# Kernel tuning notes

Measured on AMD Instinct MI355X. Metric: run time of the kernel, lower is better.

## Reference

```python
import jax, jax.numpy as jnp
import numpy as np

GRID_SIZE = 5
SPLINE_ORDER = 3
GRID_RANGE = (-1.0, 1.0)


def _make_grid():
    # knots: arange(-k, grid_size + k + 1) * h + lo -> 12 points for k=3, g=5
    h = (GRID_RANGE[1] - GRID_RANGE[0]) / GRID_SIZE
    return jnp.arange(-SPLINE_ORDER, GRID_SIZE + SPLINE_ORDER + 1, dtype=jnp.float32) * h + GRID_RANGE[0]


def _b_splines(x, grid):
    # x: (B, in) -> bases: (B, in, grid_size + spline_order) via Cox-de Boor
    x = x[..., None]  # (B, in, 1)
    bases = ((x >= grid[:-1]) & (x < grid[1:])).astype(x.dtype)
    for k in range(1, SPLINE_ORDER + 1):
        left = (x - grid[: -(k + 1)]) / (grid[k:-1] - grid[: -(k + 1)])
        right = (grid[k + 1:] - x) / (grid[k + 1:] - grid[1:-k])
        bases = left * bases[..., :-1] + right * bases[..., 1:]
    return bases


def _kan_linear(x, base_w, spline_w, spline_scaler, grid):
    # base path: SiLU(x) @ base_w.T
    base = jnp.einsum('bi,oi->bo', jax.nn.silu(x), base_w)
    # spline path: bases (B,in,K) contracted with scaled spline weight (out,in,K)
    bases = _b_splines(x, grid)
    scaled = spline_w * spline_scaler[..., None]
    spline = jnp.einsum('bik,oik->bo', bases, scaled)
    return base + spline


def setup_inputs() -> dict:
    key = jax.random.key(0)
    ks = jax.random.split(key, 9)
    B, D_in, H0, H1, L = 4096, 1024, 2048, 1024, 512
    K = GRID_SIZE + SPLINE_ORDER  # 8
    s = 0.05
    return {
        'x': jax.random.normal(ks[0], (B, D_in), jnp.float32),
        'bw0': jax.random.normal(ks[1], (H0, D_in), jnp.float32) * s,
        'sw0': jax.random.normal(ks[2], (H0, D_in, K), jnp.float32) * s,
        'ss0': jax.random.normal(ks[3], (H0, D_in), jnp.float32) * s,
        'bw1': jax.random.normal(ks[4], (H1, H0), jnp.float32) * s,
        'sw1': jax.random.normal(ks[5], (H1, H0, K), jnp.float32) * s,
        'ss1': jax.random.normal(ks[6], (H1, H0), jnp.float32) * s,
        'dw': jax.random.normal(ks[7], (L, H1), jnp.float32) * s,
        'db': jax.random.normal(ks[8], (L,), jnp.float32) * s,
    }


def reference(x, bw0, sw0, ss0, bw1, sw1, ss1, dw, db):
    grid = _make_grid()
    h = _kan_linear(x, bw0, sw0, ss0, grid)
    h = _kan_linear(h, bw1, sw1, ss1, grid)
    h = jax.nn.relu(h)
    return jnp.einsum('bi,oi->bo', h, dw) + db
```

## Files before the change

kernel.cpp:

```cpp
#include <hip/hip_runtime.h>
#include <cstdint>
#include <cstddef>


typedef __bf16 bf16x8 __attribute__((ext_vector_type(8)));
typedef __bf16 bf16x4v __attribute__((ext_vector_type(4)));
typedef float floatx4 __attribute__((ext_vector_type(4)));

#define BATCH 4096
#define DIN   1024
#define H0N   2048
#define H1N   1024
#define LOUT  512

#define OFF_A0  ((size_t)0)
#define OFF_W0  ((size_t)75497472)
#define OFF_A1  ((size_t)0)
#define OFF_P0  ((size_t)150994944)
#define OFF_W1  ((size_t)218103808)
#define OFF_P1  ((size_t)150994944)
#define OFF_H1R ((size_t)218103808)
#define OFF_DW  ((size_t)226492416)

__device__ __forceinline__ void bspline8(float x, float* out) {
    float b[11];
#pragma unroll
    for (int j = 0; j < 11; ++j) {
        float t0 = (j - 3) * 0.4f - 1.0f;
        float t1 = (j - 2) * 0.4f - 1.0f;
        b[j] = (x >= t0 && x < t1) ? 1.0f : 0.0f;
    }
#pragma unroll
    for (int k = 1; k <= 3; ++k) {
#pragma unroll
        for (int j = 0; j + k < 11; ++j) {
            float tj   = (j - 3) * 0.4f - 1.0f;
            float tj1  = (j - 2) * 0.4f - 1.0f;
            float tjk  = (j + k - 3) * 0.4f - 1.0f;
            float tjk1 = (j + k - 2) * 0.4f - 1.0f;
            float left  = (x - tj)   * (1.0f / (tjk - tj));
            float right = (tjk1 - x) * (1.0f / (tjk1 - tj1));
            b[j] = left * b[j] + right * b[j + 1];
        }
    }
#pragma unroll
    for (int j = 0; j < 8; ++j) out[j] = b[j];
}

__device__ __forceinline__ void coalesced_store9(__bf16* block_dst, const __bf16* vals) {
    __shared__ __bf16 sbuf[256 * 9];
    __bf16* p = &sbuf[threadIdx.x * 9];
#pragma unroll
    for (int j = 0; j < 9; ++j) p[j] = vals[j];
    __syncthreads();
    const uint4* src = (const uint4*)sbuf;
    uint4* dst = (uint4*)block_dst;
    dst[threadIdx.x] = src[threadIdx.x];
    if (threadIdx.x < 32) dst[256 + threadIdx.x] = src[256 + threadIdx.x];
}

__device__ __forceinline__ void act9(float v, __bf16* r) {
    float s = v / (1.0f + __expf(-v));
    float bb[8];
    bspline8(v, bb);
    r[0] = (__bf16)s;
#pragma unroll
    for (int j = 0; j < 8; ++j) r[1 + j] = (__bf16)bb[j];
}

__global__ void kan_act(const float* __restrict__ in, __bf16* __restrict__ out) {
    int base = blockIdx.x * 256;
    float v = in[base + threadIdx.x];
    __bf16 r[9];
    act9(v, r);
    coalesced_store9(out + (size_t)base * 9, r);
}

__global__ void kan_act_sum2(const __bf16* __restrict__ pa, const __bf16* __restrict__ pb,
                             __bf16* __restrict__ out) {
    int base = blockIdx.x * 256;
    int idx = base + threadIdx.x;
    float v = (float)pa[idx] + (float)pb[idx];
    __bf16 r[9];
    act9(v, r);
    coalesced_store9(out + (size_t)base * 9, r);
}

__global__ void relu_sum4(const __bf16* __restrict__ p, size_t stride,
                          __bf16* __restrict__ out, int total4) {
    int idx = blockIdx.x * 256 + threadIdx.x;
    if (idx >= total4) return;
    const bf16x4v* p0 = (const bf16x4v*)p;
    const bf16x4v* p1 = (const bf16x4v*)(p + stride);
    const bf16x4v* p2 = (const bf16x4v*)(p + 2 * stride);
    const bf16x4v* p3 = (const bf16x4v*)(p + 3 * stride);
    bf16x4v a = p0[idx], b = p1[idx], c = p2[idx], d = p3[idx];
    __bf16 r[4];
#pragma unroll
    for (int j = 0; j < 4; ++j) {
        float s = (float)a[j] + (float)b[j] + (float)c[j] + (float)d[j];
        r[j] = (__bf16)fmaxf(s, 0.0f);
    }
    *(uint2*)&out[(size_t)idx * 4] = *(uint2*)r;
}

__global__ void kan_wprep(const float* __restrict__ bw, const float* __restrict__ sw,
                          const float* __restrict__ ss, __bf16* __restrict__ out) {
    int base = blockIdx.x * 256;
    int idx = base + threadIdx.x;
    float b  = bw[idx];
    float sc = ss[idx];
    const float4* sv = (const float4*)(sw + (size_t)idx * 8);
    float4 a = sv[0], c = sv[1];
    __bf16 r[9];
    r[0] = (__bf16)b;
    r[1] = (__bf16)(a.x * sc); r[2] = (__bf16)(a.y * sc);
    r[3] = (__bf16)(a.z * sc); r[4] = (__bf16)(a.w * sc);
    r[5] = (__bf16)(c.x * sc); r[6] = (__bf16)(c.y * sc);
    r[7] = (__bf16)(c.z * sc); r[8] = (__bf16)(c.w * sc);
    coalesced_store9(out + (size_t)base * 9, r);
}

__global__ void f2bf(const float* __restrict__ in, __bf16* __restrict__ out,
                     int total) {
    int idx = blockIdx.x * 256 + threadIdx.x;
    if (idx < total) out[idx] = (__bf16)in[idx];
}

__device__ __forceinline__ void gload_lds16(const void* g, void* l) {
    __builtin_amdgcn_global_load_lds(
        (const __attribute__((address_space(1))) uint32_t*)g,
        (__attribute__((address_space(3))) uint32_t*)l, 16, 0, 0);
}


__global__ __launch_bounds__(256, 2) void gemm_pipe(
    const __bf16* __restrict__ A, const __bf16* __restrict__ W,
    __bf16* __restrict__ Cout, int M, int N, int K, int Ks) {
    constexpr int BK = 32;
    __shared__ __bf16 As[3][256 * BK];
    __shared__ __bf16 Ws[3][128 * BK];

    const int tid  = threadIdx.x;
    const int lane = tid & 63;
    const int wave = tid >> 6;

    const int id    = (blockIdx.z * gridDim.y + blockIdx.y) * gridDim.x + blockIdx.x;
    const int mslab = gridDim.y >> 3;
    const int xcd   = id & 7;
    const int local = id >> 3;
    const int m_off = local % mslab;
    const int rest  = local / mslab;
    const int ntile = rest % gridDim.x;
    const int zt    = rest / gridDim.x;
    const int bm    = (xcd * mslab + m_off) * 256;
    const int bn    = ntile * 128;
    const int kbase = zt * Ks;

    const int wm = wave * 64;
    const int lr = lane & 15;
    const int kq = lane >> 4;
    const int kssw = (kq ^ ((lr >> 1) & 3)) * 8;

    floatx4 acc[4][8] = {};

    auto stage = [&](int slot, int kstep) {
        const int kpos = kstep * BK;
#pragma unroll
        for (int i = 0; i < 4; ++i) {
            int c = i * 256 + tid;
            int r = c >> 2;
            int q = (c & 3) ^ ((r >> 1) & 3);
            gload_lds16(&A[(size_t)(bm + r) * K + kbase + kpos + q * 8],
                        &As[slot][(size_t)(i * 256 + wave * 64) * 8]);
        }
#pragma unroll
        for (int i = 0; i < 2; ++i) {
            int c = i * 256 + tid;
            int r = c >> 2;
            int q = (c & 3) ^ ((r >> 1) & 3);
            gload_lds16(&W[(size_t)(bn + r) * K + kbase + kpos + q * 8],
                        &Ws[slot][(size_t)(i * 256 + wave * 64) * 8]);
        }
    };

    auto compute = [&](int slot) {
        bf16x8 af[4], wf[8];
#pragma unroll
        for (int t = 0; t < 4; ++t)
            af[t] = *(const bf16x8*)&As[slot][(wm + t * 16 + lr) * BK + kssw];
#pragma unroll
        for (int t = 0; t < 8; ++t)
            wf[t] = *(const bf16x8*)&Ws[slot][(t * 16 + lr) * BK + kssw];
        __builtin_amdgcn_s_setprio(1);
#pragma unroll
        for (int mt = 0; mt < 4; ++mt)
#pragma unroll
            for (int nt = 0; nt < 8; ++nt)
                acc[mt][nt] = __builtin_amdgcn_mfma_f32_16x16x32_bf16(
                    af[mt], wf[nt], acc[mt][nt], 0, 0, 0);
        __builtin_amdgcn_s_setprio(0);
    };

    const int NKs = Ks >> 5;

    stage(0, 0);
    stage(1, 1);
    asm volatile("s_waitcnt vmcnt(6)" ::: "memory");
    __builtin_amdgcn_s_barrier();

    int sl = 0;
#pragma unroll 1
    for (int s = 0; s < NKs - 2; ++s) {
        int sln = sl + 2; if (sln >= 3) sln -= 3;
        stage(sln, s + 2);
        compute(sl);
        asm volatile("s_waitcnt vmcnt(6) lgkmcnt(0)" ::: "memory");
        __builtin_amdgcn_s_barrier();
        sl = (sl == 2) ? 0 : sl + 1;
    }
    compute(sl);
    asm volatile("s_waitcnt vmcnt(0) lgkmcnt(0)" ::: "memory");
    __builtin_amdgcn_s_barrier();
    sl = (sl == 2) ? 0 : sl + 1;
    compute(sl);

    __bf16* Cz = Cout + (size_t)zt * M * N;
    const int col = lane & 15;
    const int rquad = (lane >> 4) * 4;
#pragma unroll
    for (int mt = 0; mt < 4; ++mt) {
#pragma unroll
        for (int nt = 0; nt < 8; ++nt) {
            int n = bn + nt * 16 + col;
#pragma unroll
            for (int rg = 0; rg < 4; ++rg) {
                int m = bm + wm + mt * 16 + rquad + rg;
                Cz[(size_t)m * N + n] = (__bf16)acc[mt][nt][rg];
            }
        }
    }
}

__global__ __launch_bounds__(256) void gemm_dense(
    const __bf16* __restrict__ A, const __bf16* __restrict__ W,
    float* __restrict__ Cout, const float* __restrict__ bias,
    int M, int N, int K) {
    constexpr int BK = 32;
    __shared__ __bf16 As[2][128 * BK];
    __shared__ __bf16 Ws[2][128 * BK];

    const int tid  = threadIdx.x;
    const int lane = tid & 63;
    const int wave = tid >> 6;

    const int id    = blockIdx.y * gridDim.x + blockIdx.x;
    const int mslab = gridDim.y >> 3;
    const int xcd   = id & 7;
    const int local = id >> 3;
    const int m_off = local % mslab;
    const int ntile = local / mslab;
    const int bm    = (xcd * mslab + m_off) * 128;
    const int bn    = ntile * 128;

    const int wm = (wave >> 1) * 64;
    const int wn = (wave & 1) * 64;
    const int lr = lane & 15;
    const int kq = lane >> 4;
    const int kssw = (kq ^ ((lr >> 1) & 3)) * 8;

    floatx4 acc[4][4] = {};

    auto stage = [&](int buf, int kpos) {
#pragma unroll
        for (int i = 0; i < 2; ++i) {
            int c = i * 256 + tid;
            int r = c >> 2;
            int q = (c & 3) ^ ((r >> 1) & 3);
            gload_lds16(&A[(size_t)(bm + r) * K + kpos + q * 8],
                        &As[buf][(size_t)(i * 256 + wave * 64) * 8]);
            gload_lds16(&W[(size_t)(bn + r) * K + kpos + q * 8],
                        &Ws[buf][(size_t)(i * 256 + wave * 64) * 8]);
        }
    };

    auto compute = [&](int buf) {
        bf16x8 af[4], wf[4];
#pragma unroll
        for (int t = 0; t < 4; ++t) {
            af[t] = *(const bf16x8*)&As[buf][(wm + t * 16 + lr) * BK + kssw];
            wf[t] = *(const bf16x8*)&Ws[buf][(wn + t * 16 + lr) * BK + kssw];
        }
#pragma unroll
        for (int mt = 0; mt < 4; ++mt)
#pragma unroll
            for (int nt = 0; nt < 4; ++nt)
                acc[mt][nt] = __builtin_amdgcn_mfma_f32_16x16x32_bf16(
                    af[mt], wf[nt], acc[mt][nt], 0, 0, 0);
    };

    stage(0, 0);
    for (int k0 = 0; k0 < K; k0 += 2 * BK) {
        __syncthreads();
        if (k0 + BK < K) stage(1, k0 + BK);
        compute(0);
        __syncthreads();
        if (k0 + 2 * BK < K) stage(0, k0 + 2 * BK);
        compute(1);
    }

    const int col = lane & 15;
    const int rquad = (lane >> 4) * 4;
#pragma unroll
    for (int mt = 0; mt < 4; ++mt) {
#pragma unroll
        for (int nt = 0; nt < 4; ++nt) {
            int n = bn + wn + nt * 16 + col;
#pragma unroll
            for (int rg = 0; rg < 4; ++rg) {
                int m = bm + wm + mt * 16 + rquad + rg;
                Cout[(size_t)m * N + n] = acc[mt][nt][rg] + bias[n];
            }
        }
    }
}

extern "C" void kernel_launch(void* const* d_in, const int* in_sizes, int n_in,
                              void* d_out, int out_size, void* d_ws, size_t ws_size,
                              hipStream_t stream) {
    const float* x   = (const float*)d_in[0];
    const float* bw0 = (const float*)d_in[1];
    const float* sw0 = (const float*)d_in[2];
    const float* ss0 = (const float*)d_in[3];
    const float* bw1 = (const float*)d_in[4];
    const float* sw1 = (const float*)d_in[5];
    const float* ss1 = (const float*)d_in[6];
    const float* dw  = (const float*)d_in[7];
    const float* db  = (const float*)d_in[8];
    float* out = (float*)d_out;

    char* ws = (char*)d_ws;
    __bf16* A0  = (__bf16*)(ws + OFF_A0);
    __bf16* W0  = (__bf16*)(ws + OFF_W0);
    __bf16* A1  = (__bf16*)(ws + OFF_A1);
    __bf16* P0  = (__bf16*)(ws + OFF_P0);
    __bf16* W1  = (__bf16*)(ws + OFF_W1);
    __bf16* P1  = (__bf16*)(ws + OFF_P1);
    __bf16* h1r = (__bf16*)(ws + OFF_H1R);
    __bf16* dwb = (__bf16*)(ws + OFF_DW);

    kan_wprep<<<(H0N * DIN) / 256, 256, 0, stream>>>(bw0, sw0, ss0, W0);
    kan_act<<<(BATCH * DIN) / 256, 256, 0, stream>>>(x, A0);
    gemm_pipe<<<dim3(H0N / 128, BATCH / 256, 2), 256, 0, stream>>>(
        A0, W0, P0, BATCH, H0N, DIN * 9, DIN * 9 / 2);

    kan_wprep<<<(H1N * H0N) / 256, 256, 0, stream>>>(bw1, sw1, ss1, W1);
    kan_act_sum2<<<(BATCH * H0N) / 256, 256, 0, stream>>>(
        P0, P0 + (size_t)BATCH * H0N, A1);
    gemm_pipe<<<dim3(H1N / 128, BATCH / 256, 4), 256, 0, stream>>>(
        A1, W1, P1, BATCH, H1N, H0N * 9, H0N * 9 / 4);

    relu_sum4<<<(BATCH * H1N / 4) / 256, 256, 0, stream>>>(
        P1, (size_t)BATCH * H1N, h1r, BATCH * H1N / 4);

    f2bf<<<(LOUT * H1N) / 256, 256, 0, stream>>>(dw, dwb, LOUT * H1N);
    gemm_dense<<<dim3(LOUT / 128, BATCH / 128), 256, 0, stream>>>(
        h1r, dwb, out, db, BATCH, LOUT, H1N);
}
```

Measured before the change: 597.7 us.

## Replace KAN GEMM with 256x256 tile, 8-wave, BK=64 phased double-buffered kernel

The split-K bf16 GEMM used for both KAN layers moves from a 256x128 tile with 4 waves, BK=32 and triple buffering to a 256x256 tile with 8 waves (2x4 layout), BK=64 and double buffering. Each k-step is split into four MFMA phases separated by barriers, and the loads for the next A and W tiles are issued inside the first two phases. An 8-way XOR swizzle replaces the old 4-way one. The larger tile raises arithmetic intensity and reduces global traffic per FLOP, but it uses more LDS (128KB per block), launches fewer blocks, and adds barriers that may limit occupancy and latency hiding.

```diff
diff --git a/kernel.cpp b/kernel.cpp
--- a/kernel.cpp
+++ b/kernel.cpp
@@ -133,17 +133,17 @@
         (__attribute__((address_space(3))) uint32_t*)l, 16, 0, 0);
 }
 
-
-__global__ __launch_bounds__(256, 2) void gemm_pipe(
+__global__ __launch_bounds__(512, 2) void gemm8p(
     const __bf16* __restrict__ A, const __bf16* __restrict__ W,
     __bf16* __restrict__ Cout, int M, int N, int K, int Ks) {
-    constexpr int BK = 32;
-    __shared__ __bf16 As[3][256 * BK];
-    __shared__ __bf16 Ws[3][128 * BK];
+    __shared__ __bf16 As[2][256 * 64];
+    __shared__ __bf16 Ws[2][256 * 64];
 
     const int tid  = threadIdx.x;
     const int lane = tid & 63;
     const int wave = tid >> 6;
+    const int wr   = wave >> 2;
+    const int wc   = wave & 3;
 
     const int id    = (blockIdx.z * gridDim.y + blockIdx.y) * gridDim.x + blockIdx.x;
     const int mslab = gridDim.y >> 3;
@@ -154,89 +154,154 @@
     const int ntile = rest % gridDim.x;
     const int zt    = rest / gridDim.x;
     const int bm    = (xcd * mslab + m_off) * 256;
-    const int bn    = ntile * 128;
+    const int bn    = ntile * 256;
     const int kbase = zt * Ks;
 
-    const int wm = wave * 64;
+    const int srow   = wave * 8 + (lane >> 3);
+    const int schunk = (lane & 7) ^ (lane >> 3);
+
     const int lr = lane & 15;
     const int kq = lane >> 4;
-    const int kssw = (kq ^ ((lr >> 1) & 3)) * 8;
-
-    floatx4 acc[4][8] = {};
-
-    auto stage = [&](int slot, int kstep) {
-        const int kpos = kstep * BK;
-#pragma unroll
-        for (int i = 0; i < 4; ++i) {
-            int c = i * 256 + tid;
-            int r = c >> 2;
-            int q = (c & 3) ^ ((r >> 1) & 3);
-            gload_lds16(&A[(size_t)(bm + r) * K + kbase + kpos + q * 8],
-                        &As[slot][(size_t)(i * 256 + wave * 64) * 8]);
-        }
-#pragma unroll
-        for (int i = 0; i < 2; ++i) {
-            int c = i * 256 + tid;
-            int r = c >> 2;
-            int q = (c & 3) ^ ((r >> 1) & 3);
-            gload_lds16(&W[(size_t)(bn + r) * K + kbase + kpos + q * 8],
-                        &Ws[slot][(size_t)(i * 256 + wave * 64) * 8]);
+    const int swz_lo = kq ^ (lr & 7);
+
+    floatx4 acc[8][4] = {};
+
+    auto stageA = [&](int buf, int t) {
+#pragma unroll
+        for (int g = 0; g < 4; ++g) {
+            gload_lds16(&A[(size_t)(bm + g * 64 + srow) * K + kbase + t * 64 + schunk * 8],
+                        &As[buf][(size_t)(g * 64 + wave * 8) * 64]);
         }
     };
-
-    auto compute = [&](int slot) {
-        bf16x8 af[4], wf[8];
-#pragma unroll
-        for (int t = 0; t < 4; ++t)
-            af[t] = *(const bf16x8*)&As[slot][(wm + t * 16 + lr) * BK + kssw];
-#pragma unroll
-        for (int t = 0; t < 8; ++t)
-            wf[t] = *(const bf16x8*)&Ws[slot][(t * 16 + lr) * BK + kssw];
-        __builtin_amdgcn_s_setprio(1);
-#pragma unroll
-        for (int mt = 0; mt < 4; ++mt)
-#pragma unroll
-            for (int nt = 0; nt < 8; ++nt)
-                acc[mt][nt] = __builtin_amdgcn_mfma_f32_16x16x32_bf16(
-                    af[mt], wf[nt], acc[mt][nt], 0, 0, 0);
-        __builtin_amdgcn_s_setprio(0);
+    auto stageW = [&](int buf, int t) {
+#pragma unroll
+        for (int g = 0; g < 4; ++g) {
+            gload_lds16(&W[(size_t)(bn + g * 64 + srow) * K + kbase + t * 64 + schunk * 8],
+                        &Ws[buf][(size_t)(g * 64 + wave * 8) * 64]);
+        }
     };
 
-    const int NKs = Ks >> 5;
-
-    stage(0, 0);
-    stage(1, 1);
-    asm volatile("s_waitcnt vmcnt(6)" ::: "memory");
+    const int NT = Ks >> 6;
+
+    stageA(0, 0);
+    stageW(0, 0);
+    asm volatile("s_waitcnt vmcnt(0)" ::: "memory");
     __builtin_amdgcn_s_barrier();
 
-    int sl = 0;
+    int buf = 0;
 #pragma unroll 1
-    for (int s = 0; s < NKs - 2; ++s) {
-        int sln = sl + 2; if (sln >= 3) sln -= 3;
-        stage(sln, s + 2);
-        compute(sl);
-        asm volatile("s_waitcnt vmcnt(6) lgkmcnt(0)" ::: "memory");
-        __builtin_amdgcn_s_barrier();
-        sl = (sl == 2) ? 0 : sl + 1;
-    }
-    compute(sl);
-    asm volatile("s_waitcnt vmcnt(0) lgkmcnt(0)" ::: "memory");
-    __builtin_amdgcn_s_barrier();
-    sl = (sl == 2) ? 0 : sl + 1;
-    compute(sl);
+    for (int t = 0; t < NT; ++t) {
+        const bool st = (t + 1 < NT);
+        bf16x8 wf0[4], wf1[4];
+
+        {
+            bf16x8 af[4];
+            const int cs = swz_lo * 8;
+#pragma unroll
+            for (int ft = 0; ft < 4; ++ft)
+                af[ft] = *(const bf16x8*)&As[buf][(wr * 128 + ft * 16 + lr) * 64 + ((kq ^ ((lr & 7))) * 8)];
+#pragma unroll
+            for (int nt = 0; nt < 4; ++nt)
+                wf0[nt] = *(const bf16x8*)&Ws[buf][(wc * 64 + nt * 16 + lr) * 64 + cs];
+            if (st) stageA(buf ^ 1, t + 1);
+            __builtin_amdgcn_s_barrier();
+            asm volatile("s_waitcnt lgkmcnt(0)" ::: "memory");
+            __builtin_amdgcn_sched_barrier(0);
+            __builtin_amdgcn_s_setprio(1);
+#pragma unroll
+            for (int ft = 0; ft < 4; ++ft)
+#pragma unroll
+                for (int nt = 0; nt < 4; ++nt)
+                    acc[ft][nt] = __builtin_amdgcn_mfma_f32_16x16x32_bf16(
+                        af[ft], wf0[nt], acc[ft][nt], 0, 0, 0);
+            __builtin_amdgcn_s_setprio(0);
+            __builtin_amdgcn_sched_barrier(0);
+            __builtin_amdgcn_s_barrier();
+        }
+
+        {
+            bf16x8 af[4];
+            const int cs = ((4 + kq) ^ (lr & 7)) * 8;
+#pragma unroll
+            for (int ft = 0; ft < 4; ++ft)
+                af[ft] = *(const bf16x8*)&As[buf][(wr * 128 + ft * 16 + lr) * 64 + cs];
+#pragma unroll
+            for (int nt = 0; nt < 4; ++nt)
+                wf1[nt] = *(const bf16x8*)&Ws[buf][(wc * 64 + nt * 16 + lr) * 64 + cs];
+            if (st) stageW(buf ^ 1, t + 1);
+            __builtin_amdgcn_s_barrier();
+            asm volatile("s_waitcnt lgkmcnt(0)" ::: "memory");
+            __builtin_amdgcn_sched_barrier(0);
+            __builtin_amdgcn_s_setprio(1);
+#pragma unroll
+            for (int ft = 0; ft < 4; ++ft)
+#pragma unroll
+                for (int nt = 0; nt < 4; ++nt)
+                    acc[ft][nt] = __builtin_amdgcn_mfma_f32_16x16x32_bf16(
+                        af[ft], wf1[nt], acc[ft][nt], 0, 0, 0);
+            __builtin_amdgcn_s_setprio(0);
+            __builtin_amdgcn_sched_barrier(0);
+            __builtin_amdgcn_s_barrier();
+        }
+
+        {
+            bf16x8 af[4];
+            const int cs = (kq ^ (lr & 7)) * 8;
+#pragma unroll
+            for (int ft = 0; ft < 4; ++ft)
+                af[ft] = *(const bf16x8*)&As[buf][(wr * 128 + 64 + ft * 16 + lr) * 64 + cs];
+            __builtin_amdgcn_s_barrier();
+            asm volatile("s_waitcnt lgkmcnt(0)" ::: "memory");
+            __builtin_amdgcn_sched_barrier(0);
+            __builtin_amdgcn_s_setprio(1);
+#pragma unroll
+            for (int ft = 0; ft < 4; ++ft)
+#pragma unroll
+                for (int nt = 0; nt < 4; ++nt)
+                    acc[4 + ft][nt] = __builtin_amdgcn_mfma_f32_16x16x32_bf16(
+                        af[ft], wf0[nt], acc[4 + ft][nt], 0, 0, 0);
+            __builtin_amdgcn_s_setprio(0);
+            __builtin_amdgcn_sched_barrier(0);
+            __builtin_amdgcn_s_barrier();
+        }
+
+        {
+            bf16x8 af[4];
+            const int cs = ((4 + kq) ^ (lr & 7)) * 8;
+#pragma unroll
+            for (int ft = 0; ft < 4; ++ft)
+                af[ft] = *(const bf16x8*)&As[buf][(wr * 128 + 64 + ft * 16 + lr) * 64 + cs];
+            __builtin_amdgcn_s_barrier();
+            asm volatile("s_waitcnt lgkmcnt(0)" ::: "memory");
+            __builtin_amdgcn_sched_barrier(0);
+            __builtin_amdgcn_s_setprio(1);
+#pragma unroll
+            for (int ft = 0; ft < 4; ++ft)
+#pragma unroll
+                for (int nt = 0; nt < 4; ++nt)
+                    acc[4 + ft][nt] = __builtin_amdgcn_mfma_f32_16x16x32_bf16(
+                        af[ft], wf1[nt], acc[4 + ft][nt], 0, 0, 0);
+            __builtin_amdgcn_s_setprio(0);
+            __builtin_amdgcn_sched_barrier(0);
+            asm volatile("s_waitcnt vmcnt(0)" ::: "memory");
+            __builtin_amdgcn_s_barrier();
+        }
+
+        buf ^= 1;
+    }
 
     __bf16* Cz = Cout + (size_t)zt * M * N;
     const int col = lane & 15;
     const int rquad = (lane >> 4) * 4;
 #pragma unroll
-    for (int mt = 0; mt < 4; ++mt) {
-#pragma unroll
-        for (int nt = 0; nt < 8; ++nt) {
-            int n = bn + nt * 16 + col;
+    for (int mf = 0; mf < 8; ++mf) {
+#pragma unroll
+        for (int nt = 0; nt < 4; ++nt) {
+            int n = bn + wc * 64 + nt * 16 + col;
 #pragma unroll
             for (int rg = 0; rg < 4; ++rg) {
-                int m = bm + wm + mt * 16 + rquad + rg;
-                Cz[(size_t)m * N + n] = (__bf16)acc[mt][nt][rg];
+                int m = bm + wr * 128 + mf * 16 + rquad + rg;
+                Cz[(size_t)m * N + n] = (__bf16)acc[mf][nt][rg];
             }
         }
     }
@@ -351,13 +416,13 @@
 
     kan_wprep<<<(H0N * DIN) / 256, 256, 0, stream>>>(bw0, sw0, ss0, W0);
     kan_act<<<(BATCH * DIN) / 256, 256, 0, stream>>>(x, A0);
-    gemm_pipe<<<dim3(H0N / 128, BATCH / 256, 2), 256, 0, stream>>>(
+    gemm8p<<<dim3(H0N / 256, BATCH / 256, 2), 512, 0, stream>>>(
         A0, W0, P0, BATCH, H0N, DIN * 9, DIN * 9 / 2);
 
     kan_wprep<<<(H1N * H0N) / 256, 256, 0, stream>>>(bw1, sw1, ss1, W1);
     kan_act_sum2<<<(BATCH * H0N) / 256, 256, 0, stream>>>(
         P0, P0 + (size_t)BATCH * H0N, A1);
-    gemm_pipe<<<dim3(H1N / 128, BATCH / 256, 4), 256, 0, stream>>>(
+    gemm8p<<<dim3(H1N / 256, BATCH / 256, 4), 512, 0, stream>>>(
         A1, W1, P1, BATCH, H1N, H0N * 9, H0N * 9 / 4);
 
     relu_sum4<<<(BATCH * H1N / 4) / 256, 256, 0, stream>>>(
```

Measured after the change: 570.0 us. 4.6% less time.
